# Optimization experiments

Hardware: AMD Instinct MI355X
Metric: run time of the kernel (lower is better)

Reference implementation:

```python
import jax, jax.numpy as jnp
import numpy as np

# dims: N patches, D_IN input feats, D model, DI=inner, DS=state, DC=conv, DTR=dt_rank
N, D_IN, D, DI, DS, DC, DTR, NC, NL = 4096, 1024, 512, 1024, 16, 4, 32, 4, 2


def setup_inputs() -> dict:
    key = jax.random.key(0)
    ks = jax.random.split(key, 16)
    g = lambda i, shape, s=0.02: jax.random.normal(ks[i], shape, dtype=jnp.float32) * s
    return {
        "data_s": jax.random.normal(ks[0], (N, 512), dtype=jnp.float32),
        "data_l": jax.random.normal(ks[1], (N, 512), dtype=jnp.float32),
        "coord_s": jax.random.uniform(ks[2], (N, 2), dtype=jnp.float32) * 1000.0,
        "label": jax.random.randint(ks[3], (1,), 0, NC),
        "fc1_w": g(4, (D, D_IN)), "fc1_b": jnp.zeros((D,), jnp.float32),
        "ln_w": jnp.ones((NL, D), jnp.float32), "ln_b": jnp.zeros((NL, D), jnp.float32),
        "in_proj_w": g(5, (NL, 2 * DI, D)),
        "conv_w": g(6, (NL, DI, DC), 0.1), "conv_b": jnp.zeros((NL, DI), jnp.float32),
        "x_proj_w": g(7, (NL, DTR + 2 * DS, DI)),
        "dt_proj_w": g(8, (NL, DI, DTR), 0.1), "dt_proj_b": g(9, (NL, DI), 0.5),
        "A_log": jnp.broadcast_to(jnp.log(jnp.arange(1, DS + 1, dtype=jnp.float32)), (NL, DI, DS)) + jnp.zeros((NL, DI, DS), jnp.float32),
        "D_param": jnp.ones((NL, DI), jnp.float32),
        "out_proj_w": g(10, (NL, D, DI)),
        "norm_w": jnp.ones((D,), jnp.float32), "norm_b": jnp.zeros((D,), jnp.float32),
        "attn_w1": g(11, (128, D)), "attn_b1": jnp.zeros((128,), jnp.float32),
        "attn_w2": g(12, (1, 128)), "attn_b2": jnp.zeros((1,), jnp.float32),
        "cls_w": g(13, (NC, D)), "cls_b": jnp.zeros((NC,), jnp.float32),
    }


def _layer_norm(x, w, b, eps=1e-5):
    m = x.mean(-1, keepdims=True)
    v = ((x - m) ** 2).mean(-1, keepdims=True)
    return (x - m) * jax.lax.rsqrt(v + eps) * w + b


def _mamba(h, inw, cw, cb, xpw, dtw, dtb, Alog, Dp, ow):
    # h: (B, L, D) -> (B, L, D); canonical Mamba block (mamba_ssm defaults)
    B, L, _ = h.shape
    xz = h @ inw.T                      # (B, L, 2*DI)
    x, z = jnp.split(xz, 2, axis=-1)
    # causal depthwise conv1d, kernel DC, left pad DC-1 (== torch pad+truncate)
    xp = jnp.pad(x, ((0, 0), (DC - 1, 0), (0, 0)))
    x = sum(xp[:, k:k + L, :] * cw[:, k] for k in range(DC)) + cb
    x = jax.nn.silu(x)
    xdbl = x @ xpw.T                    # (B, L, DTR + 2*DS)
    dt, Bm, Cm = jnp.split(xdbl, [DTR, DTR + DS], axis=-1)
    dt = jax.nn.softplus(dt @ dtw.T + dtb)   # (B, L, DI)
    A = -jnp.exp(Alog)                  # (DI, DS)
    dA = jnp.exp(dt[..., None] * A)                          # (B, L, DI, DS)
    dBx = dt[..., None] * Bm[:, :, None, :] * x[..., None]   # (B, L, DI, DS)

    def step(hst, inp):
        dA_t, dBx_t, C_t = inp
        hst = dA_t * hst + dBx_t        # (B, DI, DS)
        return hst, jnp.einsum('bds,bs->bd', hst, C_t)

    h0 = jnp.zeros((B, DI, DS), x.dtype)
    _, ys = jax.lax.scan(step, h0, (jnp.swapaxes(dA, 0, 1), jnp.swapaxes(dBx, 0, 1), jnp.swapaxes(Cm, 0, 1)))
    y = jnp.swapaxes(ys, 0, 1) + Dp * x
    return (y * jax.nn.silu(z)) @ ow.T


def _forward(data_s, data_l, coord_s, fc1_w, fc1_b, ln_w, ln_b, in_proj_w, conv_w, conv_b,
             x_proj_w, dt_proj_w, dt_proj_b, A_log, D_param, out_proj_w, norm_w, norm_b,
             attn_w1, attn_b1, attn_w2, attn_b2, cls_w, cls_b, label):
    h = jnp.concatenate([data_s, data_l], axis=1)            # (N, 1024)
    packed = jnp.concatenate([h, coord_s], axis=1)[None]     # (1, N, 1026)
    h = packed[:, :, :-2]                                    # strip coords
    h = jax.nn.relu(h @ fc1_w.T + fc1_b)                     # dropout: eval mode (identity)
    for i in range(NL):
        res = h
        hn = _layer_norm(h, ln_w[i], ln_b[i])
        h = _mamba(hn, in_proj_w[i], conv_w[i], conv_b[i], x_proj_w[i], dt_proj_w[i],
                   dt_proj_b[i], A_log[i], D_param[i], out_proj_w[i]) + res
    h = _layer_norm(h, norm_w, norm_b)
    A = jnp.tanh(h @ attn_w1.T + attn_b1) @ attn_w2.T + attn_b2   # (1, N, 1)
    A = jax.nn.softmax(jnp.swapaxes(A, 1, 2), axis=-1)            # (1, 1, N)
    hp = (A @ h)[0]                                               # (1, D)
    logits = hp @ cls_w.T + cls_b                                 # (1, NC)
    hz = jax.nn.sigmoid(logits)
    p = jnp.clip(hz, 1e-6, 1.0 - 1e-6)
    lce = jnp.log(p) - jnp.log1p(-p)                              # torch.logit
    Y_prob = jax.nn.softmax(lce, axis=1)
    loss = -jnp.take(jax.nn.log_softmax(lce, axis=1)[0], label[0])
    return lce, Y_prob, loss


def reference(data_s, data_l, coord_s, label, fc1_w, fc1_b, ln_w, ln_b, in_proj_w, conv_w,
              conv_b, x_proj_w, dt_proj_w, dt_proj_b, A_log, D_param, out_proj_w, norm_w,
              norm_b, attn_w1, attn_b1, attn_w2, attn_b2, cls_w, cls_b):
    return _forward(data_s, data_l, coord_s, fc1_w, fc1_b, ln_w, ln_b, in_proj_w, conv_w,
                    conv_b, x_proj_w, dt_proj_w, dt_proj_b, A_log, D_param, out_proj_w,
                    norm_w, norm_b, attn_w1, attn_b1, attn_w2, attn_b2, cls_w, cls_b, label)
```

## Files before the change

### kernel.cpp

```cpp
#include <hip/hip_runtime.h>
#include <math.h>

#define L_SEQ 4096
#define DMODEL 512
#define DIN    1024
#define DI     1024
#define DS     16
#define DC     4
#define DTR    32
#define NCHK   512
#define CL     8
#define NPAIR  (DI * DS)
#define NG     32
#define GS     16
#define SLAB   (L_SEQ * 64)

typedef __bf16 bf16x8 __attribute__((ext_vector_type(8)));
typedef __bf16 bf16x4 __attribute__((ext_vector_type(4)));
typedef float floatx4 __attribute__((ext_vector_type(4)));

#define RLN2 1.44269504f
#define LN2  0.69314718f

__device__ __forceinline__ float softplus_fast(float x) {
    if (x > 20.f) return x;
    float e = __builtin_amdgcn_exp2f(x * RLN2);
    return LN2 * __builtin_amdgcn_logf(1.f + e);
}

__device__ __forceinline__ void gl2lds16(const __bf16* g, __bf16* l) {
    __builtin_amdgcn_global_load_lds(
        (const __attribute__((address_space(1))) void*)g,
        (__attribute__((address_space(3))) void*)l, 16, 0, 0);
}

template <int BN, int ACT, bool BIAS, bool ADDDEST, bool OUTBF, int KS>
__global__ __launch_bounds__(256) void gemm_mfma(
    const __bf16* __restrict__ A, int lda,
    const __bf16* __restrict__ W, int ldw,
    const float* __restrict__ bias,
    float* __restrict__ C, __bf16* __restrict__ Cb, int ldc, int K)
{
    __shared__ __align__(16) __bf16 sA[128 * 32];
    __shared__ __align__(16) __bf16 sB[BN * 32];
    const int tid = threadIdx.x;
    const int wid = tid >> 6, lane = tid & 63;
    const int m0 = blockIdx.y * 128;
    int n0;
    if (KS > 1) {
        const int ksl = blockIdx.x;
        A += (size_t)ksl * K;
        W += (size_t)ksl * K;
        C += (size_t)ksl * (size_t)gridDim.y * 128 * ldc;
        n0 = 0;
    } else {
        n0 = blockIdx.x * BN;
    }

    constexpr int MR = (BN == 128) ? 4 : 2;
    constexpr int NR = 4;
    const int wrow = (BN == 128) ? (wid >> 1) * 64 : wid * 32;
    const int wcol = (BN == 128) ? (wid & 1) * 64 : 0;

    const int srowA0 = wid * 32 + (lane >> 2);
    const int scol   = (lane & 3) * 8;
    const __bf16* aSrc0 = A + (size_t)(m0 + srowA0) * lda + scol;
    const __bf16* aSrc1 = aSrc0 + 16 * (size_t)lda;
    __bf16* aDst0 = &sA[wid * 1024];
    __bf16* aDst1 = &sA[wid * 1024 + 512];

    const __bf16* bSrc0;
    const __bf16* bSrc1 = nullptr;
    __bf16* bDst0;
    __bf16* bDst1 = nullptr;
    if (BN == 128) {
        bSrc0 = W + (size_t)(n0 + wid * 32 + (lane >> 2)) * ldw + scol;
        bSrc1 = bSrc0 + 16 * (size_t)ldw;
        bDst0 = &sB[wid * 1024];
        bDst1 = &sB[wid * 1024 + 512];
    } else {
        bSrc0 = W + (size_t)(n0 + wid * 16 + (lane >> 2)) * ldw + scol;
        bDst0 = &sB[wid * 512];
    }

    floatx4 acc[MR][NR] = {};
    const int fr = lane & 15;
    const int fk = (lane >> 4) * 8;

    for (int k0 = 0; k0 < K; k0 += 32) {
        __syncthreads();
        gl2lds16(aSrc0 + k0, aDst0);
        gl2lds16(aSrc1 + k0, aDst1);
        gl2lds16(bSrc0 + k0, bDst0);
        if (BN == 128) gl2lds16(bSrc1 + k0, bDst1);
        __syncthreads();
        bf16x8 af[MR], bfv[NR];
#pragma unroll
        for (int i = 0; i < MR; ++i)
            af[i] = *(const bf16x8*)&sA[(wrow + i * 16 + fr) * 32 + fk];
#pragma unroll
        for (int j = 0; j < NR; ++j)
            bfv[j] = *(const bf16x8*)&sB[(wcol + j * 16 + fr) * 32 + fk];
#pragma unroll
        for (int i = 0; i < MR; ++i)
#pragma unroll
            for (int j = 0; j < NR; ++j)
                acc[i][j] = __builtin_amdgcn_mfma_f32_16x16x32_bf16(
                    af[i], bfv[j], acc[i][j], 0, 0, 0);
    }

#pragma unroll
    for (int i = 0; i < MR; ++i)
#pragma unroll
        for (int j = 0; j < NR; ++j) {
            const int n = n0 + wcol + j * 16 + fr;
            float bv = 0.f;
            if (BIAS) bv = bias[n];
#pragma unroll
            for (int r = 0; r < 4; ++r) {
                const int m = m0 + wrow + i * 16 + (lane >> 4) * 4 + r;
                float v = acc[i][j][r] + bv;
                if (ACT == 1) v = fmaxf(v, 0.f);
                else if (ACT == 2) v = tanhf(v);
                const size_t idx = (size_t)m * ldc + n;
                if (OUTBF) {
                    Cb[idx] = (__bf16)v;
                } else {
                    if (ADDDEST) v += C[idx];
                    C[idx] = v;
                }
            }
        }
}

__global__ void prep_k(const float* __restrict__ s0, __bf16* __restrict__ d0, int n0,
                       const float* __restrict__ s1, __bf16* __restrict__ d1, int n1,
                       const float* __restrict__ s2, __bf16* __restrict__ d2, int n2,
                       const float* __restrict__ s3, __bf16* __restrict__ d3, int n3,
                       const float* __restrict__ s4, __bf16* __restrict__ d4, int n4,
                       const float* __restrict__ dtw, float* __restrict__ dtwT, int n5)
{
    int i = blockIdx.x * 256 + threadIdx.x;
    int tot = n0 + n1 + n2 + n3 + n4;
    if (i >= tot) {
        int j = i - tot;
        if (j < n5) {
            int l = j >> 15, rem = j & 32767, r = rem >> 5, k = rem & 31;
            dtwT[l * 32768 + k * 1024 + r] = dtw[j];
        }
        return;
    }
    const float* s; __bf16* d; int base;
    if (i < n0) { s = s0; d = d0; base = i; }
    else if (i < n0 + n1) { s = s1; d = d1; base = i - n0; }
    else if (i < n0 + n1 + n2) { s = s2; d = d2; base = i - n0 - n1; }
    else if (i < n0 + n1 + n2 + n3) { s = s3; d = d3; base = i - n0 - n1 - n2; }
    else { s = s4; d = d4; base = i - n0 - n1 - n2 - n3; }
    float4 a = ((const float4*)s)[2 * base], b = ((const float4*)s)[2 * base + 1];
    bf16x8 v;
    v[0] = (__bf16)a.x; v[1] = (__bf16)a.y; v[2] = (__bf16)a.z; v[3] = (__bf16)a.w;
    v[4] = (__bf16)b.x; v[5] = (__bf16)b.y; v[6] = (__bf16)b.z; v[7] = (__bf16)b.w;
    *(bf16x8*)&d[8 * base] = v;
}

__global__ void concat_bf_k(const float* __restrict__ a,
                            const float* __restrict__ b,
                            __bf16* __restrict__ o)
{
    int idx = blockIdx.x * 256 + threadIdx.x;
    int m = idx >> 7, c8 = (idx & 127) << 3;
    const float* src = (c8 < 512) ? &a[(m << 9) + c8] : &b[(m << 9) + c8 - 512];
    float4 x = ((const float4*)src)[0], y = ((const float4*)src)[1];
    bf16x8 v;
    v[0] = (__bf16)x.x; v[1] = (__bf16)x.y; v[2] = (__bf16)x.z; v[3] = (__bf16)x.w;
    v[4] = (__bf16)y.x; v[5] = (__bf16)y.y; v[6] = (__bf16)y.z; v[7] = (__bf16)y.w;
    *(bf16x8*)&o[idx << 3] = v;
}

template <int OMODE>
__global__ __launch_bounds__(128) void layernorm_k(
    const float* __restrict__ X, const float* __restrict__ w,
    const float* __restrict__ b, float* __restrict__ Yf, __bf16* __restrict__ Yb)
{
    const int r = blockIdx.x, tid = threadIdx.x;
    const size_t base = ((size_t)r << 9) + (tid << 2);
    const float4 v = *(const float4*)&X[base];
    float s = v.x + v.y + v.z + v.w;
#pragma unroll
    for (int o = 32; o; o >>= 1) s += __shfl_down(s, o, 64);
    __shared__ float red[2];
    if ((tid & 63) == 0) red[tid >> 6] = s;
    __syncthreads();
    const float mean = (red[0] + red[1]) * (1.f / 512.f);
    float dx = v.x - mean, dy = v.y - mean, dz = v.z - mean, dw = v.w - mean;
    float q = dx * dx + dy * dy + dz * dz + dw * dw;
#pragma unroll
    for (int o = 32; o; o >>= 1) q += __shfl_down(q, o, 64);
    __shared__ float red2[2];
    if ((tid & 63) == 0) red2[tid >> 6] = q;
    __syncthreads();
    const float rs = rsqrtf((red2[0] + red2[1]) * (1.f / 512.f) + 1e-5f);
    const float4 wv = *(const float4*)&w[tid << 2];
    const float4 bv = *(const float4*)&b[tid << 2];
    float o0 = dx * rs * wv.x + bv.x;
    float o1 = dy * rs * wv.y + bv.y;
    float o2 = dz * rs * wv.z + bv.z;
    float o3 = dw * rs * wv.w + bv.w;
    if (OMODE != 1) {
        float4 ov; ov.x = o0; ov.y = o1; ov.z = o2; ov.w = o3;
        *(float4*)&Yf[base] = ov;
    }
    if (OMODE != 0) {
        bf16x4 ov; ov[0] = (__bf16)o0; ov[1] = (__bf16)o1;
        ov[2] = (__bf16)o2; ov[3] = (__bf16)o3;
        *(bf16x4*)&Yb[base] = ov;
    }
}

__global__ void conv_silu_k(const __bf16* __restrict__ XZb,
                            const float* __restrict__ cw,
                            const float* __restrict__ cb,
                            __bf16* __restrict__ XCb)
{
    int i = blockIdx.x * 256 + threadIdx.x;
    int t = i >> 8, d4 = (i & 255) << 2;
    float wt[4][4];
#pragma unroll
    for (int d = 0; d < 4; ++d) {
        float4 w = *(const float4*)&cw[(d4 + d) << 2];
        wt[d][0] = w.x; wt[d][1] = w.y; wt[d][2] = w.z; wt[d][3] = w.w;
    }
    float4 c = *(const float4*)&cb[d4];
    float a0 = c.x, a1 = c.y, a2 = c.z, a3 = c.w;
#pragma unroll
    for (int k = 0; k < 4; ++k) {
        int ts = t + k - 3;
        if (ts >= 0) {
            bf16x4 x = *(const bf16x4*)&XZb[((size_t)ts << 11) + d4];
            a0 = fmaf((float)x[0], wt[0][k], a0);
            a1 = fmaf((float)x[1], wt[1][k], a1);
            a2 = fmaf((float)x[2], wt[2][k], a2);
            a3 = fmaf((float)x[3], wt[3][k], a3);
        }
    }
    a0 *= 1.f / (1.f + __expf(-a0));
    a1 *= 1.f / (1.f + __expf(-a1));
    a2 *= 1.f / (1.f + __expf(-a2));
    a3 *= 1.f / (1.f + __expf(-a3));
    bf16x4 ob; ob[0] = (__bf16)a0; ob[1] = (__bf16)a1;
    ob[2] = (__bf16)a2; ob[3] = (__bf16)a3;
    *(bf16x4*)&XCb[((size_t)t << 10) + d4] = ob;
}

__global__ __launch_bounds__(256) void scanA_k(
    const __bf16* __restrict__ xc, const float* __restrict__ xdblP,
    const float* __restrict__ dtwT, const float* __restrict__ dtb,
    const float* __restrict__ Alog,
    __bf16* __restrict__ sP, __bf16* __restrict__ sH,
    __bf16* __restrict__ dtg)
{
    const int d = blockIdx.x * 256 + threadIdx.x;
    const int c = blockIdx.y;
    const int tid = threadIdx.x;
    __shared__ float xlow[CL][DTR];
    __shared__ float Bs[CL][DS];
    __shared__ float dts[CL][256];
    {
        int t = tid >> 5, k = tid & 31;
        size_t g = (size_t)(c * CL + t) * 64 + k;
        xlow[t][k] = xdblP[g] + xdblP[SLAB + g] + xdblP[2 * SLAB + g] + xdblP[3 * SLAB + g];
    }
    if (tid < CL * DS) {
        int t = tid >> 4, s = tid & 15;
        size_t g = (size_t)(c * CL + t) * 64 + 32 + s;
        Bs[t][s] = xdblP[g] + xdblP[SLAB + g] + xdblP[2 * SLAB + g] + xdblP[3 * SLAB + g];
    }
    __syncthreads();
    float dtw_d[32];
#pragma unroll
    for (int k = 0; k < 32; ++k) dtw_d[k] = dtwT[k * 1024 + d];
    const float dtb_d = dtb[d];
    float sumdt = 0.f;
#pragma unroll
    for (int t = 0; t < CL; ++t) {
        float p0 = 0.f, p1 = 0.f, p2 = 0.f, p3 = 0.f;
#pragma unroll
        for (int k4 = 0; k4 < 8; ++k4) {
            float4 xq = *(const float4*)&xlow[t][k4 * 4];
            p0 = fmaf(xq.x, dtw_d[k4 * 4 + 0], p0);
            p1 = fmaf(xq.y, dtw_d[k4 * 4 + 1], p1);
            p2 = fmaf(xq.z, dtw_d[k4 * 4 + 2], p2);
            p3 = fmaf(xq.w, dtw_d[k4 * 4 + 3], p3);
        }
        float acc = ((p0 + p1) + (p2 + p3)) + dtb_d;
        float dtv = softplus_fast(acc);
        dts[t][tid] = dtv;
        dtg[((size_t)(c * CL + t) << 10) + d] = (__bf16)dtv;
        sumdt += dtv;
    }
    float As2[DS], h[DS];
    {
        const float4* Ap4 = (const float4*)&Alog[(size_t)d * DS];
#pragma unroll
        for (int q = 0; q < 4; ++q) {
            float4 a = Ap4[q];
            As2[q * 4 + 0] = -__expf(a.x) * RLN2; As2[q * 4 + 1] = -__expf(a.y) * RLN2;
            As2[q * 4 + 2] = -__expf(a.z) * RLN2; As2[q * 4 + 3] = -__expf(a.w) * RLN2;
        }
    }
#pragma unroll
    for (int s = 0; s < DS; ++s) h[s] = 0.f;
    for (int t = 0; t < CL; ++t) {
        float dtv = dts[t][tid];
        float xv = (float)xc[((size_t)(c * CL + t) << 10) + d];
        float dx = dtv * xv;
        float barr[16];
#pragma unroll
        for (int q = 0; q < 4; ++q) {
            float4 b = *(const float4*)&Bs[t][q * 4];
            barr[q * 4 + 0] = b.x; barr[q * 4 + 1] = b.y;
            barr[q * 4 + 2] = b.z; barr[q * 4 + 3] = b.w;
        }
#pragma unroll
        for (int s = 0; s < DS; ++s) {
            float a = exp2f(dtv * As2[s]);
            h[s] = fmaf(a, h[s], dx * barr[s]);
        }
    }
    size_t base = ((size_t)c * DI + d) * DS;
    bf16x8 p0v, p1v, h0v, h1v;
#pragma unroll
    for (int s = 0; s < 8; ++s) {
        p0v[s] = (__bf16)exp2f(As2[s] * sumdt);
        p1v[s] = (__bf16)exp2f(As2[s + 8] * sumdt);
        h0v[s] = (__bf16)h[s];
        h1v[s] = (__bf16)h[s + 8];
    }
    *(bf16x8*)&sP[base] = p0v; *(bf16x8*)&sP[base + 8] = p1v;
    *(bf16x8*)&sH[base] = h0v; *(bf16x8*)&sH[base + 8] = h1v;
}

__global__ __launch_bounds__(256) void scanB1_k(
    const __bf16* __restrict__ sP, const __bf16* __restrict__ sH,
    __bf16* __restrict__ PG, __bf16* __restrict__ HG)
{
    int p = blockIdx.x * 256 + threadIdx.x;
    int g = blockIdx.y;
    float rp = 1.f, rh = 0.f;
#pragma unroll
    for (int k = 0; k < GS; ++k) {
        size_t idx = (size_t)(g * GS + k) * NPAIR + p;
        float P = (float)sP[idx], H = (float)sH[idx];
        rh = fmaf(P, rh, H);
        rp *= P;
    }
    PG[(size_t)g * NPAIR + p] = (__bf16)rp;
    HG[(size_t)g * NPAIR + p] = (__bf16)rh;
}

__global__ __launch_bounds__(256) void scanB2_k(
    const __bf16* __restrict__ PG, const __bf16* __restrict__ HG,
    __bf16* __restrict__ Gin)
{
    int p = blockIdx.x * 256 + threadIdx.x;
    float run = 0.f;
#pragma unroll
    for (int g = 0; g < NG; ++g) {
        size_t idx = (size_t)g * NPAIR + p;
        Gin[idx] = (__bf16)run;
        run = fmaf((float)PG[idx], run, (float)HG[idx]);
    }
}

__global__ __launch_bounds__(256) void scanB3_k(
    const __bf16* __restrict__ sP, const __bf16* __restrict__ sH,
    const __bf16* __restrict__ Gin, __bf16* __restrict__ Hin)
{
    int p = blockIdx.x * 256 + threadIdx.x;
    int g = blockIdx.y;
    float run = (float)Gin[(size_t)g * NPAIR + p];
#pragma unroll
    for (int k = 0; k < GS; ++k) {
        size_t idx = (size_t)(g * GS + k) * NPAIR + p;
        Hin[idx] = (__bf16)run;
        run = fmaf((float)sP[idx], run, (float)sH[idx]);
    }
}

__global__ __launch_bounds__(256) void scanC_k(
    const __bf16* __restrict__ xc, const float* __restrict__ xdblP,
    const __bf16* __restrict__ dtg,
    const float* __restrict__ Alog, const float* __restrict__ Dp,
    const __bf16* __restrict__ XZb, const __bf16* __restrict__ Hin,
    __bf16* __restrict__ yz)
{
    const int d = blockIdx.x * 256 + threadIdx.x;
    const int c = blockIdx.y;
    const int tid = threadIdx.x;
    __shared__ float Bs[CL][DS], Cs[CL][DS];
    if (tid < CL * DS) {
        int t = tid >> 4, s = tid & 15;
        size_t g = (size_t)(c * CL + t) * 64 + 32 + s;
        Bs[t][s] = xdblP[g] + xdblP[SLAB + g] + xdblP[2 * SLAB + g] + xdblP[3 * SLAB + g];
        g += 16;
        Cs[t][s] = xdblP[g] + xdblP[SLAB + g] + xdblP[2 * SLAB + g] + xdblP[3 * SLAB + g];
    }
    __syncthreads();
    float As2[DS], h[DS];
    {
        const float4* Ap4 = (const float4*)&Alog[(size_t)d * DS];
#pragma unroll
        for (int q = 0; q < 4; ++q) {
            float4 a = Ap4[q];
            As2[q * 4 + 0] = -__expf(a.x) * RLN2; As2[q * 4 + 1] = -__expf(a.y) * RLN2;
            As2[q * 4 + 2] = -__expf(a.z) * RLN2; As2[q * 4 + 3] = -__expf(a.w) * RLN2;
        }
    }
    {
        size_t base = ((size_t)c * DI + d) * DS;
        bf16x8 h0 = *(const bf16x8*)&Hin[base];
        bf16x8 h1 = *(const bf16x8*)&Hin[base + 8];
#pragma unroll
        for (int s = 0; s < 8; ++s) { h[s] = (float)h0[s]; h[s + 8] = (float)h1[s]; }
    }
    const float Dd = Dp[d];
    for (int t = 0; t < CL; ++t) {
        size_t tg = (size_t)(c * CL + t);
        const float dtv = (float)dtg[(tg << 10) + d];
        const float xv = (float)xc[(tg << 10) + d];
        const float dx = dtv * xv;
        float barr[16], carr[16];
#pragma unroll
        for (int q = 0; q < 4; ++q) {
            float4 b = *(const float4*)&Bs[t][q * 4];
            float4 cc = *(const float4*)&Cs[t][q * 4];
            barr[q * 4 + 0] = b.x; barr[q * 4 + 1] = b.y;
            barr[q * 4 + 2] = b.z; barr[q * 4 + 3] = b.w;
            carr[q * 4 + 0] = cc.x; carr[q * 4 + 1] = cc.y;
            carr[q * 4 + 2] = cc.z; carr[q * 4 + 3] = cc.w;
        }
        float y = 0.f;
#pragma unroll
        for (int s = 0; s < DS; ++s) {
            float a = exp2f(dtv * As2[s]);
            h[s] = fmaf(a, h[s], dx * barr[s]);
            y = fmaf(h[s], carr[s], y);
        }
        y = fmaf(Dd, xv, y);
        float zv = (float)XZb[(tg << 11) + 1024 + d];
        float sg = 1.f / (1.f + __expf(-zv));
        yz[(tg << 10) + d] = (__bf16)(y * (zv * sg));
    }
}

__global__ void score_k(const float* __restrict__ At,
                        const float* __restrict__ w2,
                        const float* __restrict__ b2,
                        float* __restrict__ sc)
{
    int t = blockIdx.x * 256 + threadIdx.x;
    const float4* a = (const float4*)(At + ((size_t)t << 7));
    const float4* w = (const float4*)w2;
    float acc = 0.f;
#pragma unroll
    for (int j = 0; j < 32; ++j) {
        float4 av = a[j], wv = w[j];
        acc += av.x * wv.x + av.y * wv.y + av.z * wv.z + av.w * wv.w;
    }
    sc[t] = acc + b2[0];
}

__global__ __launch_bounds__(256) void softmax_k(const float* __restrict__ s,
                                                 float* __restrict__ p)
{
    const int tid = threadIdx.x;
    float vals[16];
#pragma unroll
    for (int i = 0; i < 4; ++i) {
        float4 v = *(const float4*)&s[(tid << 4) + (i << 2)];
        vals[i * 4 + 0] = v.x; vals[i * 4 + 1] = v.y;
        vals[i * 4 + 2] = v.z; vals[i * 4 + 3] = v.w;
    }
    float mx = -1e30f;
#pragma unroll
    for (int i = 0; i < 16; ++i) mx = fmaxf(mx, vals[i]);
#pragma unroll
    for (int o = 32; o; o >>= 1) mx = fmaxf(mx, __shfl_xor(mx, o, 64));
    __shared__ float red[4];
    if ((tid & 63) == 0) red[tid >> 6] = mx;
    __syncthreads();
    mx = fmaxf(fmaxf(red[0], red[1]), fmaxf(red[2], red[3]));
    float sum = 0.f, e[16];
#pragma unroll
    for (int i = 0; i < 16; ++i) { e[i] = __expf(vals[i] - mx); sum += e[i]; }
#pragma unroll
    for (int o = 32; o; o >>= 1) sum += __shfl_xor(sum, o, 64);
    __syncthreads();
    if ((tid & 63) == 0) red[tid >> 6] = sum;
    __syncthreads();
    sum = red[0] + red[1] + red[2] + red[3];
    float inv = 1.f / sum;
#pragma unroll
    for (int i = 0; i < 4; ++i) {
        float4 ov;
        ov.x = e[i * 4 + 0] * inv; ov.y = e[i * 4 + 1] * inv;
        ov.z = e[i * 4 + 2] * inv; ov.w = e[i * 4 + 3] * inv;
        *(float4*)&p[(tid << 4) + (i << 2)] = ov;
    }
}

__global__ void pool_partial_k(const float* __restrict__ prob,
                               const float* __restrict__ hln,
                               float* __restrict__ part)
{
    int j = blockIdx.x * 256 + threadIdx.x;
    int c = blockIdx.y;
    float acc = 0.f;
    for (int t = c * 128; t < (c + 1) * 128; ++t)
        acc = fmaf(prob[t], hln[((size_t)t << 9) + j], acc);
    part[c * 512 + j] = acc;
}

__global__ void pool_reduce_k(const float* __restrict__ part,
                              float* __restrict__ hp)
{
    int j = blockIdx.x * 256 + threadIdx.x;
    float acc = 0.f;
    for (int c = 0; c < 32; ++c) acc += part[c * 512 + j];
    hp[j] = acc;
}

__global__ __launch_bounds__(256) void final_head_k(
    const float* __restrict__ hp, const float* __restrict__ cls_w,
    const float* __restrict__ cls_b, const int* __restrict__ label,
    float* __restrict__ out)
{
    const int w = threadIdx.x >> 6, lane = threadIdx.x & 63;
    float acc = 0.f;
    for (int k = lane; k < 512; k += 64) acc += hp[k] * cls_w[w * 512 + k];
#pragma unroll
    for (int o = 32; o; o >>= 1) acc += __shfl_down(acc, o, 64);
    __shared__ float lg[4];
    if (lane == 0) lg[w] = acc + cls_b[w];
    __syncthreads();
    if (threadIdx.x == 0) {
        float lce[4];
        for (int c = 0; c < 4; ++c) {
            float z = lg[c];
            float hz = 1.f / (1.f + expf(-z));
            float pc = fminf(fmaxf(hz, 1e-6f), 1.f - 1e-6f);
            lce[c] = logf(pc) - log1pf(-pc);
        }
        float mx = fmaxf(fmaxf(lce[0], lce[1]), fmaxf(lce[2], lce[3]));
        float se = 0.f;
        for (int c = 0; c < 4; ++c) se += expf(lce[c] - mx);
        for (int c = 0; c < 4; ++c) out[c] = lce[c];
        for (int c = 0; c < 4; ++c) out[4 + c] = expf(lce[c] - mx) / se;
        int lb = label[0];
        out[8] = -(lce[lb] - mx - logf(se));
    }
}

extern "C" void kernel_launch(void* const* d_in, const int* in_sizes, int n_in,
                              void* d_out, int out_size, void* d_ws, size_t ws_size,
                              hipStream_t stream)
{
    const float* data_s   = (const float*)d_in[0];
    const float* data_l   = (const float*)d_in[1];
    const int*   label    = (const int*)d_in[3];
    const float* fc1_w    = (const float*)d_in[4];
    const float* fc1_b    = (const float*)d_in[5];
    const float* ln_w     = (const float*)d_in[6];
    const float* ln_b     = (const float*)d_in[7];
    const float* in_proj_w= (const float*)d_in[8];
    const float* conv_w   = (const float*)d_in[9];
    const float* conv_b   = (const float*)d_in[10];
    const float* x_proj_w = (const float*)d_in[11];
    const float* dt_proj_w= (const float*)d_in[12];
    const float* dt_proj_b= (const float*)d_in[13];
    const float* A_log    = (const float*)d_in[14];
    const float* D_param  = (const float*)d_in[15];
    const float* out_proj_w=(const float*)d_in[16];
    const float* norm_w   = (const float*)d_in[17];
    const float* norm_b   = (const float*)d_in[18];
    const float* attn_w1  = (const float*)d_in[19];
    const float* attn_b1  = (const float*)d_in[20];
    const float* attn_w2  = (const float*)d_in[21];
    const float* attn_b2  = (const float*)d_in[22];
    const float* cls_w    = (const float*)d_in[23];
    const float* cls_b    = (const float*)d_in[24];
    float* out = (float*)d_out;

    float* ws = (float*)d_ws;
    size_t off = 0;
    float* h     = ws + off; off += (size_t)L_SEQ * DMODEL;
    float* hn    = ws + off; off += (size_t)L_SEQ * DMODEL;
    float* xdblP = ws + off; off += (size_t)4 * SLAB;
    float* dtwT  = ws + off; off += (size_t)2 * DTR * DI;
    float* At    = ws + off; off += (size_t)L_SEQ * 128;
    float* sc    = ws + off; off += L_SEQ;
    float* pb    = ws + off; off += L_SEQ;
    float* part  = ws + off; off += 32 * 512;
    float* hp    = ws + off; off += 512;

    __bf16* bws = (__bf16*)(ws + off);
    size_t boff = 0;
    __bf16* Acatb = bws + boff; boff += (size_t)L_SEQ * DIN;
    __bf16* hnb   = bws + boff; boff += (size_t)L_SEQ * DMODEL;
    __bf16* XZb   = bws + boff; boff += (size_t)L_SEQ * 2 * DI;
    __bf16* XCb   = bws + boff; boff += (size_t)L_SEQ * DI;
    __bf16* yzb   = bws + boff; boff += (size_t)L_SEQ * DI;
    __bf16* sPb   = bws + boff; boff += (size_t)NCHK * NPAIR;
    __bf16* sHb   = bws + boff; boff += (size_t)NCHK * NPAIR;
    __bf16* HinB  = bws + boff; boff += (size_t)NCHK * NPAIR;
    __bf16* dtgB  = bws + boff; boff += (size_t)L_SEQ * DI;
    __bf16* PGb   = bws + boff; boff += (size_t)NG * NPAIR;
    __bf16* HGb   = bws + boff; boff += (size_t)NG * NPAIR;
    __bf16* GinB  = bws + boff; boff += (size_t)NG * NPAIR;
    __bf16* wfc1b = bws + boff; boff += (size_t)DMODEL * DIN;
    __bf16* winb  = bws + boff; boff += (size_t)2 * 2 * DI * DMODEL;
    __bf16* wxpb  = bws + boff; boff += (size_t)2 * 64 * DI;
    __bf16* woutb = bws + boff; boff += (size_t)2 * DMODEL * DI;
    __bf16* w1b   = bws + boff; boff += (size_t)128 * DMODEL;
    if (ws_size < off * sizeof(float) + boff * sizeof(__bf16)) return;

    const int n0 = DMODEL * DIN / 8;
    const int n1 = 2 * 2 * DI * DMODEL / 8;
    const int n2 = 2 * 64 * DI / 8;
    const int n3 = 2 * DMODEL * DI / 8;
    const int n4 = 128 * DMODEL / 8;
    const int n5 = 2 * DI * DTR;
    prep_k<<<(n0 + n1 + n2 + n3 + n4 + n5 + 255) / 256, 256, 0, stream>>>(
        fc1_w, wfc1b, n0, in_proj_w, winb, n1, x_proj_w, wxpb, n2,
        out_proj_w, woutb, n3, attn_w1, w1b, n4, dt_proj_w, dtwT, n5);

    concat_bf_k<<<L_SEQ * DIN / 8 / 256, 256, 0, stream>>>(data_s, data_l, Acatb);
    gemm_mfma<64, 1, true, false, false, 1><<<dim3(DMODEL / 64, L_SEQ / 128), 256, 0, stream>>>(
        Acatb, DIN, wfc1b, DIN, fc1_b, h, nullptr, DMODEL, DIN);

    for (int i = 0; i < 2; ++i) {
        const __bf16* inw = winb + (size_t)i * 2 * DI * DMODEL;
        const float* cwi = conv_w + (size_t)i * DI * DC;
        const float* cbi = conv_b + (size_t)i * DI;
        const __bf16* xpw = wxpb + (size_t)i * 64 * DI;
        const float* dtwTi = dtwT + (size_t)i * DTR * DI;
        const float* dtbv= dt_proj_b + (size_t)i * DI;
        const float* Alg = A_log + (size_t)i * DI * DS;
        const float* Dpi = D_param + (size_t)i * DI;
        const __bf16* owi = woutb + (size_t)i * DMODEL * DI;

        layernorm_k<1><<<L_SEQ, 128, 0, stream>>>(h, ln_w + i * DMODEL, ln_b + i * DMODEL, nullptr, hnb);
        gemm_mfma<128, 0, false, false, true, 1><<<dim3(2 * DI / 128, L_SEQ / 128), 256, 0, stream>>>(
            hnb, DMODEL, inw, DMODEL, nullptr, nullptr, XZb, 2 * DI, DMODEL);
        conv_silu_k<<<L_SEQ * DI / 4 / 256, 256, 0, stream>>>(XZb, cwi, cbi, XCb);
        gemm_mfma<64, 0, false, false, false, 4><<<dim3(4, L_SEQ / 128), 256, 0, stream>>>(
            XCb, DI, xpw, DI, nullptr, xdblP, nullptr, 64, DI / 4);
        scanA_k<<<dim3(DI / 256, NCHK), 256, 0, stream>>>(XCb, xdblP, dtwTi, dtbv, Alg, sPb, sHb, dtgB);
        scanB1_k<<<dim3(NPAIR / 256, NG), 256, 0, stream>>>(sPb, sHb, PGb, HGb);
        scanB2_k<<<NPAIR / 256, 256, 0, stream>>>(PGb, HGb, GinB);
        scanB3_k<<<dim3(NPAIR / 256, NG), 256, 0, stream>>>(sPb, sHb, GinB, HinB);
        scanC_k<<<dim3(DI / 256, NCHK), 256, 0, stream>>>(XCb, xdblP, dtgB, Alg, Dpi, XZb, HinB, yzb);
        gemm_mfma<64, 0, false, true, false, 1><<<dim3(DMODEL / 64, L_SEQ / 128), 256, 0, stream>>>(
            yzb, DI, owi, DI, nullptr, h, nullptr, DMODEL, DI);
    }

    layernorm_k<2><<<L_SEQ, 128, 0, stream>>>(h, norm_w, norm_b, hn, hnb);
    gemm_mfma<64, 2, true, false, false, 1><<<dim3(2, L_SEQ / 128), 256, 0, stream>>>(
        hnb, DMODEL, w1b, DMODEL, attn_b1, At, nullptr, 128, DMODEL);
    score_k<<<L_SEQ / 256, 256, 0, stream>>>(At, attn_w2, attn_b2, sc);
    softmax_k<<<1, 256, 0, stream>>>(sc, pb);
    pool_partial_k<<<dim3(2, 32), 256, 0, stream>>>(pb, hn, part);
    pool_reduce_k<<<2, 256, 0, stream>>>(part, hp);
    final_head_k<<<1, 256, 0, stream>>>(hp, cls_w, cls_b, label, out);
}
```

Baseline: 393.9 us.

## Compute local scan outputs in chunk pass and apply carry-in correction separately

The chunked selective scan now produces the zero-initial-state output y and the cumulative dt inside the first chunk pass. A new elementwise finish kernel adds the carried-in state contribution exp(A*cumdt)*Hin·C and applies the z gate, replacing the second full sequential recompute pass (scanC). The exp(A_log) transform is precomputed once in the prep kernel. The change removes a second per-chunk recurrence, but it adds bf16 stores and loads of yloc and cumsum and a 16-wide exp2 per element in the finish pass, which may cost some precision.

```diff
diff --git a/kernel.cpp b/kernel.cpp
--- a/kernel.cpp
+++ b/kernel.cpp
@@ -138,7 +138,8 @@
                        const float* __restrict__ s2, __bf16* __restrict__ d2, int n2,
                        const float* __restrict__ s3, __bf16* __restrict__ d3, int n3,
                        const float* __restrict__ s4, __bf16* __restrict__ d4, int n4,
-                       const float* __restrict__ dtw, float* __restrict__ dtwT, int n5)
+                       const float* __restrict__ dtw, float* __restrict__ dtwT, int n5,
+                       const float* __restrict__ Alog, float* __restrict__ As2T, int n6)
 {
     int i = blockIdx.x * 256 + threadIdx.x;
     int tot = n0 + n1 + n2 + n3 + n4;
@@ -147,6 +148,9 @@
         if (j < n5) {
             int l = j >> 15, rem = j & 32767, r = rem >> 5, k = rem & 31;
             dtwT[l * 32768 + k * 1024 + r] = dtw[j];
+        } else if (j - n5 < n6) {
+            int k = j - n5;
+            As2T[k] = -__expf(Alog[k]) * RLN2;
         }
         return;
     }
@@ -255,15 +259,15 @@
 __global__ __launch_bounds__(256) void scanA_k(
     const __bf16* __restrict__ xc, const float* __restrict__ xdblP,
     const float* __restrict__ dtwT, const float* __restrict__ dtb,
-    const float* __restrict__ Alog,
+    const float* __restrict__ As2T, const float* __restrict__ Dp,
     __bf16* __restrict__ sP, __bf16* __restrict__ sH,
-    __bf16* __restrict__ dtg)
+    __bf16* __restrict__ cums, __bf16* __restrict__ yloc)
 {
     const int d = blockIdx.x * 256 + threadIdx.x;
     const int c = blockIdx.y;
     const int tid = threadIdx.x;
     __shared__ float xlow[CL][DTR];
-    __shared__ float Bs[CL][DS];
+    __shared__ float Bs[CL][DS], Cs[CL][DS];
     __shared__ float dts[CL][256];
     {
         int t = tid >> 5, k = tid & 31;
@@ -274,6 +278,8 @@
         int t = tid >> 4, s = tid & 15;
         size_t g = (size_t)(c * CL + t) * 64 + 32 + s;
         Bs[t][s] = xdblP[g] + xdblP[SLAB + g] + xdblP[2 * SLAB + g] + xdblP[3 * SLAB + g];
+        g += 16;
+        Cs[t][s] = xdblP[g] + xdblP[SLAB + g] + xdblP[2 * SLAB + g] + xdblP[3 * SLAB + g];
     }
     __syncthreads();
     float dtw_d[32];
@@ -295,140 +301,26 @@
         float acc = ((p0 + p1) + (p2 + p3)) + dtb_d;
         float dtv = softplus_fast(acc);
         dts[t][tid] = dtv;
-        dtg[((size_t)(c * CL + t) << 10) + d] = (__bf16)dtv;
         sumdt += dtv;
+        cums[((size_t)(c * CL + t) << 10) + d] = (__bf16)sumdt;
     }
     float As2[DS], h[DS];
     {
-        const float4* Ap4 = (const float4*)&Alog[(size_t)d * DS];
+        const float4* Ap4 = (const float4*)&As2T[(size_t)d * DS];
 #pragma unroll
         for (int q = 0; q < 4; ++q) {
             float4 a = Ap4[q];
-            As2[q * 4 + 0] = -__expf(a.x) * RLN2; As2[q * 4 + 1] = -__expf(a.y) * RLN2;
-            As2[q * 4 + 2] = -__expf(a.z) * RLN2; As2[q * 4 + 3] = -__expf(a.w) * RLN2;
+            As2[q * 4 + 0] = a.x; As2[q * 4 + 1] = a.y;
+            As2[q * 4 + 2] = a.z; As2[q * 4 + 3] = a.w;
         }
     }
 #pragma unroll
     for (int s = 0; s < DS; ++s) h[s] = 0.f;
+    const float Dd = Dp[d];
     for (int t = 0; t < CL; ++t) {
         float dtv = dts[t][tid];
         float xv = (float)xc[((size_t)(c * CL + t) << 10) + d];
         float dx = dtv * xv;
-        float barr[16];
-#pragma unroll
-        for (int q = 0; q < 4; ++q) {
-            float4 b = *(const float4*)&Bs[t][q * 4];
-            barr[q * 4 + 0] = b.x; barr[q * 4 + 1] = b.y;
-            barr[q * 4 + 2] = b.z; barr[q * 4 + 3] = b.w;
-        }
-#pragma unroll
-        for (int s = 0; s < DS; ++s) {
-            float a = exp2f(dtv * As2[s]);
-            h[s] = fmaf(a, h[s], dx * barr[s]);
-        }
-    }
-    size_t base = ((size_t)c * DI + d) * DS;
-    bf16x8 p0v, p1v, h0v, h1v;
-#pragma unroll
-    for (int s = 0; s < 8; ++s) {
-        p0v[s] = (__bf16)exp2f(As2[s] * sumdt);
-        p1v[s] = (__bf16)exp2f(As2[s + 8] * sumdt);
-        h0v[s] = (__bf16)h[s];
-        h1v[s] = (__bf16)h[s + 8];
-    }
-    *(bf16x8*)&sP[base] = p0v; *(bf16x8*)&sP[base + 8] = p1v;
-    *(bf16x8*)&sH[base] = h0v; *(bf16x8*)&sH[base + 8] = h1v;
-}
-
-__global__ __launch_bounds__(256) void scanB1_k(
-    const __bf16* __restrict__ sP, const __bf16* __restrict__ sH,
-    __bf16* __restrict__ PG, __bf16* __restrict__ HG)
-{
-    int p = blockIdx.x * 256 + threadIdx.x;
-    int g = blockIdx.y;
-    float rp = 1.f, rh = 0.f;
-#pragma unroll
-    for (int k = 0; k < GS; ++k) {
-        size_t idx = (size_t)(g * GS + k) * NPAIR + p;
-        float P = (float)sP[idx], H = (float)sH[idx];
-        rh = fmaf(P, rh, H);
-        rp *= P;
-    }
-    PG[(size_t)g * NPAIR + p] = (__bf16)rp;
-    HG[(size_t)g * NPAIR + p] = (__bf16)rh;
-}
-
-__global__ __launch_bounds__(256) void scanB2_k(
-    const __bf16* __restrict__ PG, const __bf16* __restrict__ HG,
-    __bf16* __restrict__ Gin)
-{
-    int p = blockIdx.x * 256 + threadIdx.x;
-    float run = 0.f;
-#pragma unroll
-    for (int g = 0; g < NG; ++g) {
-        size_t idx = (size_t)g * NPAIR + p;
-        Gin[idx] = (__bf16)run;
-        run = fmaf((float)PG[idx], run, (float)HG[idx]);
-    }
-}
-
-__global__ __launch_bounds__(256) void scanB3_k(
-    const __bf16* __restrict__ sP, const __bf16* __restrict__ sH,
-    const __bf16* __restrict__ Gin, __bf16* __restrict__ Hin)
-{
-    int p = blockIdx.x * 256 + threadIdx.x;
-    int g = blockIdx.y;
-    float run = (float)Gin[(size_t)g * NPAIR + p];
-#pragma unroll
-    for (int k = 0; k < GS; ++k) {
-        size_t idx = (size_t)(g * GS + k) * NPAIR + p;
-        Hin[idx] = (__bf16)run;
-        run = fmaf((float)sP[idx], run, (float)sH[idx]);
-    }
-}
-
-__global__ __launch_bounds__(256) void scanC_k(
-    const __bf16* __restrict__ xc, const float* __restrict__ xdblP,
-    const __bf16* __restrict__ dtg,
-    const float* __restrict__ Alog, const float* __restrict__ Dp,
-    const __bf16* __restrict__ XZb, const __bf16* __restrict__ Hin,
-    __bf16* __restrict__ yz)
-{
-    const int d = blockIdx.x * 256 + threadIdx.x;
-    const int c = blockIdx.y;
-    const int tid = threadIdx.x;
-    __shared__ float Bs[CL][DS], Cs[CL][DS];
-    if (tid < CL * DS) {
-        int t = tid >> 4, s = tid & 15;
-        size_t g = (size_t)(c * CL + t) * 64 + 32 + s;
-        Bs[t][s] = xdblP[g] + xdblP[SLAB + g] + xdblP[2 * SLAB + g] + xdblP[3 * SLAB + g];
-        g += 16;
-        Cs[t][s] = xdblP[g] + xdblP[SLAB + g] + xdblP[2 * SLAB + g] + xdblP[3 * SLAB + g];
-    }
-    __syncthreads();
-    float As2[DS], h[DS];
-    {
-        const float4* Ap4 = (const float4*)&Alog[(size_t)d * DS];
-#pragma unroll
-        for (int q = 0; q < 4; ++q) {
-            float4 a = Ap4[q];
-            As2[q * 4 + 0] = -__expf(a.x) * RLN2; As2[q * 4 + 1] = -__expf(a.y) * RLN2;
-            As2[q * 4 + 2] = -__expf(a.z) * RLN2; As2[q * 4 + 3] = -__expf(a.w) * RLN2;
-        }
-    }
-    {
-        size_t base = ((size_t)c * DI + d) * DS;
-        bf16x8 h0 = *(const bf16x8*)&Hin[base];
-        bf16x8 h1 = *(const bf16x8*)&Hin[base + 8];
-#pragma unroll
-        for (int s = 0; s < 8; ++s) { h[s] = (float)h0[s]; h[s + 8] = (float)h1[s]; }
-    }
-    const float Dd = Dp[d];
-    for (int t = 0; t < CL; ++t) {
-        size_t tg = (size_t)(c * CL + t);
-        const float dtv = (float)dtg[(tg << 10) + d];
-        const float xv = (float)xc[(tg << 10) + d];
-        const float dx = dtv * xv;
         float barr[16], carr[16];
 #pragma unroll
         for (int q = 0; q < 4; ++q) {
@@ -447,10 +339,110 @@
             y = fmaf(h[s], carr[s], y);
         }
         y = fmaf(Dd, xv, y);
-        float zv = (float)XZb[(tg << 11) + 1024 + d];
-        float sg = 1.f / (1.f + __expf(-zv));
-        yz[(tg << 10) + d] = (__bf16)(y * (zv * sg));
-    }
+        yloc[((size_t)(c * CL + t) << 10) + d] = (__bf16)y;
+    }
+    size_t base = ((size_t)c * DI + d) * DS;
+    bf16x8 p0v, p1v, h0v, h1v;
+#pragma unroll
+    for (int s = 0; s < 8; ++s) {
+        p0v[s] = (__bf16)exp2f(As2[s] * sumdt);
+        p1v[s] = (__bf16)exp2f(As2[s + 8] * sumdt);
+        h0v[s] = (__bf16)h[s];
+        h1v[s] = (__bf16)h[s + 8];
+    }
+    *(bf16x8*)&sP[base] = p0v; *(bf16x8*)&sP[base + 8] = p1v;
+    *(bf16x8*)&sH[base] = h0v; *(bf16x8*)&sH[base + 8] = h1v;
+}
+
+__global__ __launch_bounds__(256) void scanB1_k(
+    const __bf16* __restrict__ sP, const __bf16* __restrict__ sH,
+    __bf16* __restrict__ PG, __bf16* __restrict__ HG)
+{
+    int p = blockIdx.x * 256 + threadIdx.x;
+    int g = blockIdx.y;
+    float rp = 1.f, rh = 0.f;
+#pragma unroll
+    for (int k = 0; k < GS; ++k) {
+        size_t idx = (size_t)(g * GS + k) * NPAIR + p;
+        float P = (float)sP[idx], H = (float)sH[idx];
+        rh = fmaf(P, rh, H);
+        rp *= P;
+    }
+    PG[(size_t)g * NPAIR + p] = (__bf16)rp;
+    HG[(size_t)g * NPAIR + p] = (__bf16)rh;
+}
+
+__global__ __launch_bounds__(256) void scanB2_k(
+    const __bf16* __restrict__ PG, const __bf16* __restrict__ HG,
+    __bf16* __restrict__ Gin)
+{
+    int p = blockIdx.x * 256 + threadIdx.x;
+    float run = 0.f;
+#pragma unroll
+    for (int g = 0; g < NG; ++g) {
+        size_t idx = (size_t)g * NPAIR + p;
+        Gin[idx] = (__bf16)run;
+        run = fmaf((float)PG[idx], run, (float)HG[idx]);
+    }
+}
+
+__global__ __launch_bounds__(256) void scanB3_k(
+    const __bf16* __restrict__ sP, const __bf16* __restrict__ sH,
+    const __bf16* __restrict__ Gin, __bf16* __restrict__ Hin)
+{
+    int p = blockIdx.x * 256 + threadIdx.x;
+    int g = blockIdx.y;
+    float run = (float)Gin[(size_t)g * NPAIR + p];
+#pragma unroll
+    for (int k = 0; k < GS; ++k) {
+        size_t idx = (size_t)(g * GS + k) * NPAIR + p;
+        Hin[idx] = (__bf16)run;
+        run = fmaf((float)sP[idx], run, (float)sH[idx]);
+    }
+}
+
+__global__ __launch_bounds__(256) void finish_k(
+    const __bf16* __restrict__ yloc, const __bf16* __restrict__ cums,
+    const __bf16* __restrict__ Hin, const float* __restrict__ As2T,
+    const float* __restrict__ xdblP, const __bf16* __restrict__ XZb,
+    __bf16* __restrict__ yz)
+{
+    const int tid = threadIdx.x;
+    const int idx = blockIdx.x * 256 + tid;
+    const int t = idx >> 10, d = idx & 1023;
+    const int c = t >> 3;
+    __shared__ float Cls[DS];
+    if (tid < DS) {
+        size_t g = (size_t)t * 64 + 48 + tid;
+        Cls[tid] = xdblP[g] + xdblP[SLAB + g] + xdblP[2 * SLAB + g] + xdblP[3 * SLAB + g];
+    }
+    __syncthreads();
+    const float cv = (float)cums[idx];
+    float As2[DS];
+    {
+        const float4* Ap4 = (const float4*)&As2T[(size_t)d * DS];
+#pragma unroll
+        for (int q = 0; q < 4; ++q) {
+            float4 a = Ap4[q];
+            As2[q * 4 + 0] = a.x; As2[q * 4 + 1] = a.y;
+            As2[q * 4 + 2] = a.z; As2[q * 4 + 3] = a.w;
+        }
+    }
+    float hs[DS];
+    {
+        size_t base = (size_t)c * NPAIR + (size_t)d * DS;
+        bf16x8 h0 = *(const bf16x8*)&Hin[base];
+        bf16x8 h1 = *(const bf16x8*)&Hin[base + 8];
+#pragma unroll
+        for (int s = 0; s < 8; ++s) { hs[s] = (float)h0[s]; hs[s + 8] = (float)h1[s]; }
+    }
+    float y = (float)yloc[idx];
+#pragma unroll
+    for (int s = 0; s < DS; ++s)
+        y = fmaf(exp2f(As2[s] * cv) * hs[s], Cls[s], y);
+    float zv = (float)XZb[((size_t)t << 11) + 1024 + d];
+    float sg = 1.f / (1.f + __expf(-zv));
+    yz[idx] = (__bf16)(y * (zv * sg));
 }
 
 __global__ void score_k(const float* __restrict__ At,
@@ -597,6 +589,7 @@
     float* hn    = ws + off; off += (size_t)L_SEQ * DMODEL;
     float* xdblP = ws + off; off += (size_t)4 * SLAB;
     float* dtwT  = ws + off; off += (size_t)2 * DTR * DI;
+    float* As2T  = ws + off; off += (size_t)2 * DI * DS;
     float* At    = ws + off; off += (size_t)L_SEQ * 128;
     float* sc    = ws + off; off += L_SEQ;
     float* pb    = ws + off; off += L_SEQ;
@@ -613,7 +606,8 @@
     __bf16* sPb   = bws + boff; boff += (size_t)NCHK * NPAIR;
     __bf16* sHb   = bws + boff; boff += (size_t)NCHK * NPAIR;
     __bf16* HinB  = bws + boff; boff += (size_t)NCHK * NPAIR;
-    __bf16* dtgB  = bws + boff; boff += (size_t)L_SEQ * DI;
+    __bf16* cumsB = bws + boff; boff += (size_t)L_SEQ * DI;
+    __bf16* ylocB = bws + boff; boff += (size_t)L_SEQ * DI;
     __bf16* PGb   = bws + boff; boff += (size_t)NG * NPAIR;
     __bf16* HGb   = bws + boff; boff += (size_t)NG * NPAIR;
     __bf16* GinB  = bws + boff; boff += (size_t)NG * NPAIR;
@@ -630,9 +624,11 @@
     const int n3 = 2 * DMODEL * DI / 8;
     const int n4 = 128 * DMODEL / 8;
     const int n5 = 2 * DI * DTR;
-    prep_k<<<(n0 + n1 + n2 + n3 + n4 + n5 + 255) / 256, 256, 0, stream>>>(
+    const int n6 = 2 * DI * DS;
+    prep_k<<<(n0 + n1 + n2 + n3 + n4 + n5 + n6 + 255) / 256, 256, 0, stream>>>(
         fc1_w, wfc1b, n0, in_proj_w, winb, n1, x_proj_w, wxpb, n2,
-        out_proj_w, woutb, n3, attn_w1, w1b, n4, dt_proj_w, dtwT, n5);
+        out_proj_w, woutb, n3, attn_w1, w1b, n4, dt_proj_w, dtwT, n5,
+        A_log, As2T, n6);
 
     concat_bf_k<<<L_SEQ * DIN / 8 / 256, 256, 0, stream>>>(data_s, data_l, Acatb);
     gemm_mfma<64, 1, true, false, false, 1><<<dim3(DMODEL / 64, L_SEQ / 128), 256, 0, stream>>>(
@@ -645,7 +641,7 @@
         const __bf16* xpw = wxpb + (size_t)i * 64 * DI;
         const float* dtwTi = dtwT + (size_t)i * DTR * DI;
         const float* dtbv= dt_proj_b + (size_t)i * DI;
-        const float* Alg = A_log + (size_t)i * DI * DS;
+        const float* As2i = As2T + (size_t)i * DI * DS;
         const float* Dpi = D_param + (size_t)i * DI;
         const __bf16* owi = woutb + (size_t)i * DMODEL * DI;
 
@@ -655,11 +651,13 @@
         conv_silu_k<<<L_SEQ * DI / 4 / 256, 256, 0, stream>>>(XZb, cwi, cbi, XCb);
         gemm_mfma<64, 0, false, false, false, 4><<<dim3(4, L_SEQ / 128), 256, 0, stream>>>(
             XCb, DI, xpw, DI, nullptr, xdblP, nullptr, 64, DI / 4);
-        scanA_k<<<dim3(DI / 256, NCHK), 256, 0, stream>>>(XCb, xdblP, dtwTi, dtbv, Alg, sPb, sHb, dtgB);
+        scanA_k<<<dim3(DI / 256, NCHK), 256, 0, stream>>>(
+            XCb, xdblP, dtwTi, dtbv, As2i, Dpi, sPb, sHb, cumsB, ylocB);
         scanB1_k<<<dim3(NPAIR / 256, NG), 256, 0, stream>>>(sPb, sHb, PGb, HGb);
         scanB2_k<<<NPAIR / 256, 256, 0, stream>>>(PGb, HGb, GinB);
         scanB3_k<<<dim3(NPAIR / 256, NG), 256, 0, stream>>>(sPb, sHb, GinB, HinB);
-        scanC_k<<<dim3(DI / 256, NCHK), 256, 0, stream>>>(XCb, xdblP, dtgB, Alg, Dpi, XZb, HinB, yzb);
+        finish_k<<<L_SEQ * DI / 256, 256, 0, stream>>>(
+            ylocB, cumsB, HinB, As2i, xdblP, XZb, yzb);
         gemm_mfma<64, 0, false, true, false, 1><<<dim3(DMODEL / 64, L_SEQ / 128), 256, 0, stream>>>(
             yzb, DI, owi, DI, nullptr, h, nullptr, DMODEL, DI);
     }
```

Result: slower. 408.0 us (+3.6%).

## Replace per-chunk decay array with chunk dt sums recomputed in scan passes

Applied to the files above, without the earlier changes.

The chunked scan no longer writes the per-chunk decay products sP (NCHK x DI x DS bf16). It stores one bf16 dt sum per chunk and channel, and scanB1/scanB3 recompute the decay with exp2f from that sum and a precomputed A coefficient. The -exp(A_log)/ln2 coefficients are also computed once in the prep kernel instead of in every scanA and scanC thread. This removes a large intermediate's write and two reads in exchange for extra exp2f work, and rounding the dt sum to bf16 before exponentiating can shift accuracy.

```diff
diff --git a/kernel.cpp b/kernel.cpp
--- a/kernel.cpp
+++ b/kernel.cpp
@@ -138,7 +138,8 @@
                        const float* __restrict__ s2, __bf16* __restrict__ d2, int n2,
                        const float* __restrict__ s3, __bf16* __restrict__ d3, int n3,
                        const float* __restrict__ s4, __bf16* __restrict__ d4, int n4,
-                       const float* __restrict__ dtw, float* __restrict__ dtwT, int n5)
+                       const float* __restrict__ dtw, float* __restrict__ dtwT, int n5,
+                       const float* __restrict__ Alog, float* __restrict__ As2T, int n6)
 {
     int i = blockIdx.x * 256 + threadIdx.x;
     int tot = n0 + n1 + n2 + n3 + n4;
@@ -147,6 +148,9 @@
         if (j < n5) {
             int l = j >> 15, rem = j & 32767, r = rem >> 5, k = rem & 31;
             dtwT[l * 32768 + k * 1024 + r] = dtw[j];
+        } else if (j - n5 < n6) {
+            int k = j - n5;
+            As2T[k] = -__expf(Alog[k]) * RLN2;
         }
         return;
     }
@@ -255,8 +259,8 @@
 __global__ __launch_bounds__(256) void scanA_k(
     const __bf16* __restrict__ xc, const float* __restrict__ xdblP,
     const float* __restrict__ dtwT, const float* __restrict__ dtb,
-    const float* __restrict__ Alog,
-    __bf16* __restrict__ sP, __bf16* __restrict__ sH,
+    const float* __restrict__ As2T,
+    __bf16* __restrict__ dtsum, __bf16* __restrict__ sH,
     __bf16* __restrict__ dtg)
 {
     const int d = blockIdx.x * 256 + threadIdx.x;
@@ -298,14 +302,15 @@
         dtg[((size_t)(c * CL + t) << 10) + d] = (__bf16)dtv;
         sumdt += dtv;
     }
+    dtsum[(size_t)c * DI + d] = (__bf16)sumdt;
     float As2[DS], h[DS];
     {
-        const float4* Ap4 = (const float4*)&Alog[(size_t)d * DS];
+        const float4* Ap4 = (const float4*)&As2T[(size_t)d * DS];
 #pragma unroll
         for (int q = 0; q < 4; ++q) {
             float4 a = Ap4[q];
-            As2[q * 4 + 0] = -__expf(a.x) * RLN2; As2[q * 4 + 1] = -__expf(a.y) * RLN2;
-            As2[q * 4 + 2] = -__expf(a.z) * RLN2; As2[q * 4 + 3] = -__expf(a.w) * RLN2;
+            As2[q * 4 + 0] = a.x; As2[q * 4 + 1] = a.y;
+            As2[q * 4 + 2] = a.z; As2[q * 4 + 3] = a.w;
         }
     }
 #pragma unroll
@@ -328,29 +333,30 @@
         }
     }
     size_t base = ((size_t)c * DI + d) * DS;
-    bf16x8 p0v, p1v, h0v, h1v;
+    bf16x8 h0v, h1v;
 #pragma unroll
     for (int s = 0; s < 8; ++s) {
-        p0v[s] = (__bf16)exp2f(As2[s] * sumdt);
-        p1v[s] = (__bf16)exp2f(As2[s + 8] * sumdt);
         h0v[s] = (__bf16)h[s];
         h1v[s] = (__bf16)h[s + 8];
     }
-    *(bf16x8*)&sP[base] = p0v; *(bf16x8*)&sP[base + 8] = p1v;
     *(bf16x8*)&sH[base] = h0v; *(bf16x8*)&sH[base + 8] = h1v;
 }
 
 __global__ __launch_bounds__(256) void scanB1_k(
-    const __bf16* __restrict__ sP, const __bf16* __restrict__ sH,
+    const __bf16* __restrict__ dtsum, const __bf16* __restrict__ sH,
+    const float* __restrict__ As2T,
     __bf16* __restrict__ PG, __bf16* __restrict__ HG)
 {
     int p = blockIdx.x * 256 + threadIdx.x;
     int g = blockIdx.y;
+    const int d = p >> 4;
+    const float as2 = As2T[p];
     float rp = 1.f, rh = 0.f;
 #pragma unroll
     for (int k = 0; k < GS; ++k) {
-        size_t idx = (size_t)(g * GS + k) * NPAIR + p;
-        float P = (float)sP[idx], H = (float)sH[idx];
+        int c = g * GS + k;
+        float P = exp2f(as2 * (float)dtsum[(size_t)c * DI + d]);
+        float H = (float)sH[(size_t)c * NPAIR + p];
         rh = fmaf(P, rh, H);
         rp *= P;
     }
@@ -373,26 +379,30 @@
 }
 
 __global__ __launch_bounds__(256) void scanB3_k(
-    const __bf16* __restrict__ sP, const __bf16* __restrict__ sH,
+    const __bf16* __restrict__ dtsum, const __bf16* __restrict__ sH,
+    const float* __restrict__ As2T,
     const __bf16* __restrict__ Gin, __bf16* __restrict__ Hin)
 {
     int p = blockIdx.x * 256 + threadIdx.x;
     int g = blockIdx.y;
+    const int d = p >> 4;
+    const float as2 = As2T[p];
     float run = (float)Gin[(size_t)g * NPAIR + p];
 #pragma unroll
     for (int k = 0; k < GS; ++k) {
-        size_t idx = (size_t)(g * GS + k) * NPAIR + p;
+        int c = g * GS + k;
+        size_t idx = (size_t)c * NPAIR + p;
         Hin[idx] = (__bf16)run;
-        run = fmaf((float)sP[idx], run, (float)sH[idx]);
+        float P = exp2f(as2 * (float)dtsum[(size_t)c * DI + d]);
+        run = fmaf(P, run, (float)sH[idx]);
     }
 }
 
 __global__ __launch_bounds__(256) void scanC_k(
     const __bf16* __restrict__ xc, const float* __restrict__ xdblP,
-    const __bf16* __restrict__ dtg,
-    const float* __restrict__ Alog, const float* __restrict__ Dp,
-    const __bf16* __restrict__ XZb, const __bf16* __restrict__ Hin,
-    __bf16* __restrict__ yz)
+    const __bf16* __restrict__ dtg, const float* __restrict__ As2T,
+    const float* __restrict__ Dp, const __bf16* __restrict__ XZb,
+    const __bf16* __restrict__ Hin, __bf16* __restrict__ yz)
 {
     const int d = blockIdx.x * 256 + threadIdx.x;
     const int c = blockIdx.y;
@@ -408,12 +418,12 @@
     __syncthreads();
     float As2[DS], h[DS];
     {
-        const float4* Ap4 = (const float4*)&Alog[(size_t)d * DS];
+        const float4* Ap4 = (const float4*)&As2T[(size_t)d * DS];
 #pragma unroll
         for (int q = 0; q < 4; ++q) {
             float4 a = Ap4[q];
-            As2[q * 4 + 0] = -__expf(a.x) * RLN2; As2[q * 4 + 1] = -__expf(a.y) * RLN2;
-            As2[q * 4 + 2] = -__expf(a.z) * RLN2; As2[q * 4 + 3] = -__expf(a.w) * RLN2;
+            As2[q * 4 + 0] = a.x; As2[q * 4 + 1] = a.y;
+            As2[q * 4 + 2] = a.z; As2[q * 4 + 3] = a.w;
         }
     }
     {
@@ -597,6 +607,7 @@
     float* hn    = ws + off; off += (size_t)L_SEQ * DMODEL;
     float* xdblP = ws + off; off += (size_t)4 * SLAB;
     float* dtwT  = ws + off; off += (size_t)2 * DTR * DI;
+    float* As2T  = ws + off; off += (size_t)2 * DI * DS;
     float* At    = ws + off; off += (size_t)L_SEQ * 128;
     float* sc    = ws + off; off += L_SEQ;
     float* pb    = ws + off; off += L_SEQ;
@@ -610,10 +621,10 @@
     __bf16* XZb   = bws + boff; boff += (size_t)L_SEQ * 2 * DI;
     __bf16* XCb   = bws + boff; boff += (size_t)L_SEQ * DI;
     __bf16* yzb   = bws + boff; boff += (size_t)L_SEQ * DI;
-    __bf16* sPb   = bws + boff; boff += (size_t)NCHK * NPAIR;
     __bf16* sHb   = bws + boff; boff += (size_t)NCHK * NPAIR;
     __bf16* HinB  = bws + boff; boff += (size_t)NCHK * NPAIR;
     __bf16* dtgB  = bws + boff; boff += (size_t)L_SEQ * DI;
+    __bf16* dtsumB= bws + boff; boff += (size_t)NCHK * DI;
     __bf16* PGb   = bws + boff; boff += (size_t)NG * NPAIR;
     __bf16* HGb   = bws + boff; boff += (size_t)NG * NPAIR;
     __bf16* GinB  = bws + boff; boff += (size_t)NG * NPAIR;
@@ -630,9 +641,11 @@
     const int n3 = 2 * DMODEL * DI / 8;
     const int n4 = 128 * DMODEL / 8;
     const int n5 = 2 * DI * DTR;
-    prep_k<<<(n0 + n1 + n2 + n3 + n4 + n5 + 255) / 256, 256, 0, stream>>>(
+    const int n6 = 2 * DI * DS;
+    prep_k<<<(n0 + n1 + n2 + n3 + n4 + n5 + n6 + 255) / 256, 256, 0, stream>>>(
         fc1_w, wfc1b, n0, in_proj_w, winb, n1, x_proj_w, wxpb, n2,
-        out_proj_w, woutb, n3, attn_w1, w1b, n4, dt_proj_w, dtwT, n5);
+        out_proj_w, woutb, n3, attn_w1, w1b, n4, dt_proj_w, dtwT, n5,
+        A_log, As2T, n6);
 
     concat_bf_k<<<L_SEQ * DIN / 8 / 256, 256, 0, stream>>>(data_s, data_l, Acatb);
     gemm_mfma<64, 1, true, false, false, 1><<<dim3(DMODEL / 64, L_SEQ / 128), 256, 0, stream>>>(
@@ -645,7 +658,7 @@
         const __bf16* xpw = wxpb + (size_t)i * 64 * DI;
         const float* dtwTi = dtwT + (size_t)i * DTR * DI;
         const float* dtbv= dt_proj_b + (size_t)i * DI;
-        const float* Alg = A_log + (size_t)i * DI * DS;
+        const float* As2i = As2T + (size_t)i * DI * DS;
         const float* Dpi = D_param + (size_t)i * DI;
         const __bf16* owi = woutb + (size_t)i * DMODEL * DI;
 
@@ -655,11 +668,13 @@
         conv_silu_k<<<L_SEQ * DI / 4 / 256, 256, 0, stream>>>(XZb, cwi, cbi, XCb);
         gemm_mfma<64, 0, false, false, false, 4><<<dim3(4, L_SEQ / 128), 256, 0, stream>>>(
             XCb, DI, xpw, DI, nullptr, xdblP, nullptr, 64, DI / 4);
-        scanA_k<<<dim3(DI / 256, NCHK), 256, 0, stream>>>(XCb, xdblP, dtwTi, dtbv, Alg, sPb, sHb, dtgB);
-        scanB1_k<<<dim3(NPAIR / 256, NG), 256, 0, stream>>>(sPb, sHb, PGb, HGb);
+        scanA_k<<<dim3(DI / 256, NCHK), 256, 0, stream>>>(
+            XCb, xdblP, dtwTi, dtbv, As2i, dtsumB, sHb, dtgB);
+        scanB1_k<<<dim3(NPAIR / 256, NG), 256, 0, stream>>>(dtsumB, sHb, As2i, PGb, HGb);
         scanB2_k<<<NPAIR / 256, 256, 0, stream>>>(PGb, HGb, GinB);
-        scanB3_k<<<dim3(NPAIR / 256, NG), 256, 0, stream>>>(sPb, sHb, GinB, HinB);
-        scanC_k<<<dim3(DI / 256, NCHK), 256, 0, stream>>>(XCb, xdblP, dtgB, Alg, Dpi, XZb, HinB, yzb);
+        scanB3_k<<<dim3(NPAIR / 256, NG), 256, 0, stream>>>(dtsumB, sHb, As2i, GinB, HinB);
+        scanC_k<<<dim3(DI / 256, NCHK), 256, 0, stream>>>(
+            XCb, xdblP, dtgB, As2i, Dpi, XZb, HinB, yzb);
         gemm_mfma<64, 0, false, true, false, 1><<<dim3(DMODEL / 64, L_SEQ / 128), 256, 0, stream>>>(
             yzb, DI, owi, DI, nullptr, h, nullptr, DMODEL, DI);
     }
```

Measured after the change: 405.5 us. 2.9% more time.
